# Optimization experiments

Hardware: AMD Instinct MI355X
Metric: run time of the kernel (lower is better)

Reference implementation:

```python
import jax, jax.numpy as jnp
import numpy as np

# Faithful math of the torch module (dropout in eval mode => identity):
#   alpha = sigmoid(smoothing_weight)                       # [h,1] -> [1,1,h,1]
#   out[t] = alpha^(t+1) * v0 + sum_{s<=t} (1-alpha) alpha^(t-s) * values[s]
#   aux path kernel: weight/clamp(1-alpha,1e-6)*alpha => factor*alpha^(t-s+1)
#     with factor = (1-alpha)/max(1-alpha,1e-6) (== 1 unless alpha ~ 1)
# The torch code realizes this causal linear recurrence via FFT cross-correlation;
# here we use an associative (parallel) scan, which computes the same sums.

B, T, H, D = 8, 4096, 8, 64

def setup_inputs() -> dict:
    key = jax.random.key(0)
    k1, k2, k3, k4 = jax.random.split(key, 4)
    values = jax.random.normal(k1, (B, T, H, D), dtype=jnp.float32)
    aux_values = jax.random.normal(k2, (B, T, H, D), dtype=jnp.float32)
    v0 = jax.random.normal(k3, (1, 1, H, D), dtype=jnp.float32)
    smoothing_weight = jax.random.normal(k4, (H, 1), dtype=jnp.float32)
    return {"values": values, "aux_values": aux_values, "v0": v0,
            "smoothing_weight": smoothing_weight}

def reference(values, aux_values, v0, smoothing_weight):
    b, t, h, d = values.shape
    alpha = jax.nn.sigmoid(smoothing_weight).reshape(1, 1, h, 1)  # [1,1,h,1]
    one_m = 1.0 - alpha
    factor = one_m / jnp.maximum(one_m, 1e-6)  # == 1 unless alpha ~ 1 (clamp in torch)
    # Linear recurrence y[t] = alpha*y[t-1] + u[t], y[-1] = v0, where
    # u[t] = (1-alpha)*values[t] + factor*alpha*aux_values[t] (fused main + aux path).
    a = jnp.broadcast_to(alpha, (1, t, h, 1))               # decay coeffs
    u = one_m * values + (factor * alpha) * aux_values      # [b,t,h,d]
    def combine(c1, c2):
        a1, b1 = c1
        a2, b2 = c2
        return (a1 * a2, a2 * b1 + b2)
    A, Bsum = jax.lax.associative_scan(combine, (a, u), axis=1)
    # A[t] = alpha^(t+1); Bsum[t] = sum_{s<=t} alpha^(t-s) * u[s]
    return A * v0 + Bsum
```

## Files before the change

### kernel.cpp

```cpp
#include <hip/hip_runtime.h>
#include <math.h>

#define BB 8
#define TT 4096
#define HH 8
#define DD 64
#define NC 256
#define LL (TT / NC)

__device__ __forceinline__ float sigmoidf_(float x) {
    return 1.0f / (1.0f + expf(-x));
}

__global__ __launch_bounds__(128)
void k_partial(const float4* __restrict__ vals, const float4* __restrict__ aux,
               const float* __restrict__ w, float4* __restrict__ out,
               float4* __restrict__ Z) {
    const int blk = blockIdx.x;
    const int b = blk / NC, c = blk % NC;
    const int tid = threadIdx.x;
    const int h = tid >> 4;

    const float alpha = sigmoidf_(w[h]);
    const float onem  = 1.0f - alpha;
    const float fa    = (onem / fmaxf(onem, 1e-6f)) * alpha;

    int base = (b * TT + c * LL) * 128 + tid;

    float4 y = make_float4(0.f, 0.f, 0.f, 0.f);
#pragma unroll
    for (int i = 0; i < LL; ++i) {
        float4 v = vals[base + i * 128];
        float4 a = aux[base + i * 128];
        y.x = alpha * y.x + (onem * v.x + fa * a.x);
        y.y = alpha * y.y + (onem * v.y + fa * a.y);
        y.z = alpha * y.z + (onem * v.z + fa * a.z);
        y.w = alpha * y.w + (onem * v.w + fa * a.w);
        out[base + i * 128] = y;
    }
    Z[(b * NC + c) * 128 + tid] = y;
}

__global__ __launch_bounds__(256)
void k_scan(const float4* __restrict__ Z, const float* __restrict__ v0,
            const float* __restrict__ w, float4* __restrict__ P) {
    __shared__ float lds[NC][33];

    const int blk = blockIdx.x;
    const int b  = blk >> 4;
    const int h  = (blk >> 1) & 7;
    const int dh = blk & 1;
    const int r4base = h * 16 + dh * 8;
    const int tid = threadIdx.x;

    const float alpha = sigmoidf_(w[h]);
    const float aL = powf(alpha, (float)LL);

#pragma unroll
    for (int it = 0; it < 8; ++it) {
        int idx = it * 256 + tid;
        int c = idx >> 3, k = idx & 7;
        float4 z = Z[(b * NC + c) * 128 + r4base + k];
        lds[c][k * 4 + 0] = z.x;
        lds[c][k * 4 + 1] = z.y;
        lds[c][k * 4 + 2] = z.z;
        lds[c][k * 4 + 3] = z.w;
    }
    __syncthreads();

    const int c = tid;
    float s[32];
#pragma unroll
    for (int k = 0; k < 32; ++k) s[k] = lds[c][k];

    float m = aL;
    for (int off = 1; off < NC; off <<= 1) {
        float tmp[32];
        const bool act = (c >= off);
        if (act) {
#pragma unroll
            for (int k = 0; k < 32; ++k) tmp[k] = lds[c - off][k];
        }
        __syncthreads();
        if (act) {
#pragma unroll
            for (int k = 0; k < 32; ++k) { s[k] += m * tmp[k]; lds[c][k] = s[k]; }
        }
        m *= m;
        __syncthreads();
    }

    const float pc = powf(alpha, (float)(LL * c));
    const float4* v04 = (const float4*)v0;
#pragma unroll
    for (int k = 0; k < 8; ++k) {
        float4 vv = v04[r4base + k];
        float4 pr;
        if (c == 0) {
            pr = vv;
        } else {
            pr.x = pc * vv.x + lds[c - 1][k * 4 + 0];
            pr.y = pc * vv.y + lds[c - 1][k * 4 + 1];
            pr.z = pc * vv.z + lds[c - 1][k * 4 + 2];
            pr.w = pc * vv.w + lds[c - 1][k * 4 + 3];
        }
        P[(b * NC + c) * 128 + r4base + k] = pr;
    }
}

__global__ __launch_bounds__(128)
void k_final(const float* __restrict__ w, const float4* __restrict__ P,
             float4* __restrict__ out) {
    const int blk = blockIdx.x;
    const int b = blk / NC, c = blk % NC;
    const int tid = threadIdx.x;
    const int h = tid >> 4;

    const float alpha = sigmoidf_(w[h]);
    const float4 p = P[(b * NC + c) * 128 + tid];
    int base = (b * TT + c * LL) * 128 + tid;

    float coef = alpha;
#pragma unroll
    for (int i = 0; i < LL; ++i) {
        float4 o = out[base + i * 128];
        o.x += coef * p.x;
        o.y += coef * p.y;
        o.z += coef * p.z;
        o.w += coef * p.w;
        out[base + i * 128] = o;
        coef *= alpha;
    }
}

extern "C" void kernel_launch(void* const* d_in, const int* in_sizes, int n_in,
                              void* d_out, int out_size, void* d_ws, size_t ws_size,
                              hipStream_t stream) {
    const float4* vals = (const float4*)d_in[0];
    const float4* aux  = (const float4*)d_in[1];
    const float*  v0   = (const float*)d_in[2];
    const float*  w    = (const float*)d_in[3];
    float4* out = (float4*)d_out;

    float4* Z = (float4*)d_ws;
    float4* P = Z + (size_t)BB * NC * 128;

    k_partial<<<BB * NC, 128, 0, stream>>>(vals, aux, w, out, Z);
    k_scan<<<BB * HH * 2, 256, 0, stream>>>(Z, v0, w, P);
    k_final<<<BB * NC, 128, 0, stream>>>(w, P, out);
}
```

Measured before the change: 196.5 us.

## Switch to reduce-then-scan: aggregate chunks, then recompute recurrence in final pass

Result: no change. 200.4 us (+2.0%).

```diff
diff --git a/kernel.cpp b/kernel.cpp
--- a/kernel.cpp
+++ b/kernel.cpp
@@ -5,17 +5,17 @@
 #define TT 4096
 #define HH 8
 #define DD 64
-#define NC 256
-#define LL (TT / NC)
+#define LL 16
+#define NC (TT / LL)
+#define NBLK (BB * NC)
 
 __device__ __forceinline__ float sigmoidf_(float x) {
     return 1.0f / (1.0f + expf(-x));
 }
 
 __global__ __launch_bounds__(128)
-void k_partial(const float4* __restrict__ vals, const float4* __restrict__ aux,
-               const float* __restrict__ w, float4* __restrict__ out,
-               float4* __restrict__ Z) {
+void k_agg(const float4* __restrict__ vals, const float4* __restrict__ aux,
+           const float* __restrict__ w, float4* __restrict__ Z) {
     const int blk = blockIdx.x;
     const int b = blk / NC, c = blk % NC;
     const int tid = threadIdx.x;
@@ -25,20 +25,26 @@
     const float onem  = 1.0f - alpha;
     const float fa    = (onem / fmaxf(onem, 1e-6f)) * alpha;
 
-    int base = (b * TT + c * LL) * 128 + tid;
+    const int base = (b * TT + c * LL) * 128 + tid;
 
     float4 y = make_float4(0.f, 0.f, 0.f, 0.f);
 #pragma unroll
-    for (int i = 0; i < LL; ++i) {
-        float4 v = vals[base + i * 128];
-        float4 a = aux[base + i * 128];
-        y.x = alpha * y.x + (onem * v.x + fa * a.x);
-        y.y = alpha * y.y + (onem * v.y + fa * a.y);
-        y.z = alpha * y.z + (onem * v.z + fa * a.z);
-        y.w = alpha * y.w + (onem * v.w + fa * a.w);
-        out[base + i * 128] = y;
+    for (int g = 0; g < 2; ++g) {
+        float4 v[8], a[8];
+#pragma unroll
+        for (int i = 0; i < 8; ++i) {
+            v[i] = vals[base + (g * 8 + i) * 128];
+            a[i] = aux [base + (g * 8 + i) * 128];
+        }
+#pragma unroll
+        for (int i = 0; i < 8; ++i) {
+            y.x = alpha * y.x + (onem * v[i].x + fa * a[i].x);
+            y.y = alpha * y.y + (onem * v[i].y + fa * a[i].y);
+            y.z = alpha * y.z + (onem * v[i].z + fa * a[i].z);
+            y.w = alpha * y.w + (onem * v[i].w + fa * a[i].w);
+        }
     }
-    Z[(b * NC + c) * 128 + tid] = y;
+    Z[blk * 128 + tid] = y;
 }
 
 __global__ __launch_bounds__(256)
@@ -54,17 +60,17 @@
     const int tid = threadIdx.x;
 
     const float alpha = sigmoidf_(w[h]);
-    const float aL = powf(alpha, (float)LL);
+    float aL = alpha * alpha; aL *= aL; aL *= aL; aL *= aL;
 
 #pragma unroll
     for (int it = 0; it < 8; ++it) {
         int idx = it * 256 + tid;
-        int c = idx >> 3, k = idx & 7;
-        float4 z = Z[(b * NC + c) * 128 + r4base + k];
-        lds[c][k * 4 + 0] = z.x;
-        lds[c][k * 4 + 1] = z.y;
-        lds[c][k * 4 + 2] = z.z;
-        lds[c][k * 4 + 3] = z.w;
+        int cc = idx >> 3, k = idx & 7;
+        float4 z = Z[(b * NC + cc) * 128 + r4base + k];
+        lds[cc][k * 4 + 0] = z.x;
+        lds[cc][k * 4 + 1] = z.y;
+        lds[cc][k * 4 + 2] = z.z;
+        lds[cc][k * 4 + 3] = z.w;
     }
     __syncthreads();
 
@@ -109,7 +115,8 @@
 }
 
 __global__ __launch_bounds__(128)
-void k_final(const float* __restrict__ w, const float4* __restrict__ P,
+void k_final(const float4* __restrict__ vals, const float4* __restrict__ aux,
+             const float* __restrict__ w, const float4* __restrict__ P,
              float4* __restrict__ out) {
     const int blk = blockIdx.x;
     const int b = blk / NC, c = blk % NC;
@@ -117,19 +124,28 @@
     const int h = tid >> 4;
 
     const float alpha = sigmoidf_(w[h]);
-    const float4 p = P[(b * NC + c) * 128 + tid];
-    int base = (b * TT + c * LL) * 128 + tid;
+    const float onem  = 1.0f - alpha;
+    const float fa    = (onem / fmaxf(onem, 1e-6f)) * alpha;
 
-    float coef = alpha;
+    const int base = (b * TT + c * LL) * 128 + tid;
+
+    float4 y = P[blk * 128 + tid];
 #pragma unroll
-    for (int i = 0; i < LL; ++i) {
-        float4 o = out[base + i * 128];
-        o.x += coef * p.x;
-        o.y += coef * p.y;
-        o.z += coef * p.z;
-        o.w += coef * p.w;
-        out[base + i * 128] = o;
-        coef *= alpha;
+    for (int g = 0; g < 2; ++g) {
+        float4 v[8], a[8];
+#pragma unroll
+        for (int i = 0; i < 8; ++i) {
+            v[i] = vals[base + (g * 8 + i) * 128];
+            a[i] = aux [base + (g * 8 + i) * 128];
+        }
+#pragma unroll
+        for (int i = 0; i < 8; ++i) {
+            y.x = alpha * y.x + (onem * v[i].x + fa * a[i].x);
+            y.y = alpha * y.y + (onem * v[i].y + fa * a[i].y);
+            y.z = alpha * y.z + (onem * v[i].z + fa * a[i].z);
+            y.w = alpha * y.w + (onem * v[i].w + fa * a[i].w);
+            out[base + (g * 8 + i) * 128] = y;
+        }
     }
 }
 
@@ -143,9 +159,9 @@
     float4* out = (float4*)d_out;
 
     float4* Z = (float4*)d_ws;
-    float4* P = Z + (size_t)BB * NC * 128;
+    float4* P = Z + (size_t)NBLK * 128;
 
-    k_partial<<<BB * NC, 128, 0, stream>>>(vals, aux, w, out, Z);
-    k_scan<<<BB * HH * 2, 256, 0, stream>>>(Z, v0, w, P);
-    k_final<<<BB * NC, 128, 0, stream>>>(w, P, out);
+    k_agg  <<<NBLK, 128, 0, stream>>>(vals, aux, w, Z);
+    k_scan <<<BB * HH * 2, 256, 0, stream>>>(Z, v0, w, P);
+    k_final<<<NBLK, 128, 0, stream>>>(vals, aux, w, P, out);
 }
```
